# Performance work log

Hardware: AMD Instinct MI355X
Metric: run time of the kernel (lower is better)

The kernel has to match this reference:

```python
import jax, jax.numpy as jnp
import numpy as np

NC = 128      # nc
K = 5         # cube kernel size
NS = 3        # n_scale pyramid levels
NV = 150000   # vertices (cortical-surface scale)
NF = 300000   # faces ~ 2*NV
L = 192       # volume side (L = W = H -> rescale = [1,1,1])


def setup_inputs() -> dict:
    key = jax.random.key(0)
    ks = jax.random.split(key, 16)
    s = 0.05
    return {
        "v": jax.random.uniform(ks[0], (1, NV, 3), minval=-0.9, maxval=0.9, dtype=jnp.float32),
        "f": jax.random.randint(ks[1], (1, NF, 3), 0, NV, dtype=jnp.int32),
        "volume": jax.random.normal(ks[2], (1, 1, L, L, L), dtype=jnp.float32),
        "fc1_w": jax.random.normal(ks[3], (6, NC), dtype=jnp.float32) * s,
        "fc1_b": jnp.zeros((NC,), jnp.float32),
        "fc2_w": jax.random.normal(ks[4], (2 * NC, 4 * NC), dtype=jnp.float32) * s,
        "fc2_b": jnp.zeros((4 * NC,), jnp.float32),
        "fc3_w": jax.random.normal(ks[5], (4 * NC, 2 * NC), dtype=jnp.float32) * s,
        "fc3_b": jnp.zeros((2 * NC,), jnp.float32),
        "fc4_w": jax.random.normal(ks[6], (2 * NC, 3), dtype=jnp.float32) * s,
        "fc4_b": jnp.zeros((3,), jnp.float32),
        "conv_w": jax.random.normal(ks[7], (NC, NS, K, K, K), dtype=jnp.float32) * s,
        "conv_b": jnp.zeros((NC,), jnp.float32),
        "lfc_w": jax.random.normal(ks[8], (NC, NC), dtype=jnp.float32) * s,
        "lfc_b": jnp.zeros((NC,), jnp.float32),
    }


def _vertex_normals(v, f):
    # pytorch3d-style vertex normals: scatter-add area-weighted face normals, then normalize.
    verts, faces = v[0], f[0]
    p0, p1, p2 = verts[faces[:, 0]], verts[faces[:, 1]], verts[faces[:, 2]]
    fn = jnp.cross(p1 - p0, p2 - p0)  # [NF, 3]
    n = jnp.zeros_like(verts)
    n = n.at[faces[:, 0]].add(fn).at[faces[:, 1]].add(fn).at[faces[:, 2]].add(fn)
    n = n / jnp.maximum(jnp.linalg.norm(n, axis=-1, keepdims=True), 1e-12)
    return n[None]  # [1, NV, 3]


def _cube_sampling(v, volume):
    # Vectorized version of the 125-iteration Python gather loop:
    # gather a KxKxK neighborhood per vertex at each pyramid scale.
    vol_n = volume[0, 0]
    off = jnp.arange(-(K - 1) // 2, (K - 1) // 2 + 1)  # [-2..2]
    cubes = []
    for n in range(NS):
        if n > 0:
            s = vol_n.shape[0]
            vol_n = vol_n.reshape(s // 2, 2, s // 2, 2, s // 2, 2).mean(axis=(1, 3, 5))  # avg_pool3d(2)
        idx = jnp.round((v[0] + 1.0) * L / 2 ** (n + 1)).astype(jnp.int32)  # rescale = [1,1,1]
        idx = jnp.clip(idx, (K - 1) // 2, L // 2 ** n - 3)
        i0 = idx[:, 0, None, None, None] + off[None, :, None, None]
        i1 = idx[:, 1, None, None, None] + off[None, None, :, None]
        i2 = idx[:, 2, None, None, None] + off[None, None, None, :]
        cubes.append(vol_n[i0, i1, i2])  # [NV, K, K, K]
    return jnp.stack(cubes, axis=1)  # [NV, NS, K, K, K]


def reference(v, f, volume, fc1_w, fc1_b, fc2_w, fc2_b, fc3_w, fc3_b, fc4_w, fc4_b,
              conv_w, conv_b, lfc_w, lfc_b):
    coord = v
    normal = _vertex_normals(v, f)
    x = jnp.concatenate([v, normal], axis=2)                 # [1, NV, 6]
    x = jax.nn.leaky_relu(x @ fc1_w + fc1_b, 0.15)           # [1, NV, NC]
    cubes = _cube_sampling(v, volume)                        # [NV, NS, K, K, K]
    # Conv3d with kernel == input size -> single output voxel == full contraction.
    x_local = jnp.einsum('ncijk,ocijk->no', cubes, conv_w) + conv_b  # [NV, NC]
    x_local = (x_local @ lfc_w + lfc_b)[None]                # [1, NV, NC]
    x = jnp.concatenate([x, x_local], axis=2)                # [1, NV, 2*NC]
    x = jax.nn.leaky_relu(x @ fc2_w + fc2_b, 0.15)
    x = jax.nn.leaky_relu(x @ fc3_w + fc3_b, 0.15)
    x = jnp.tanh(x @ fc4_w + fc4_b) * 0.1
    return coord + x
```

## Files before the change

### kernel.cpp

```cpp
#include <hip/hip_runtime.h>
#include <hip/hip_bf16.h>
#include <math.h>

#define NVERT 150000
#define NFACE 300000
#define LVOL  192
#define TVB   32
#define MTV   48

#define P2_POOL1 3456
#define P2_POOL2 432
#define P2_WC    193
#define P2_CP0   3456
#define P2_POOL2_START (P2_POOL1)
#define P2_WC_START    (P2_POOL1 + P2_POOL2)
#define P2_CP0_START   (P2_POOL1 + P2_POOL2 + P2_WC)

#define NB_NORM 1172
#define NB_TRS  1024

#define WS_BIG_NEED 44808576ull
#define WS_B16_NEED 58964352ull

typedef short v8s __attribute__((ext_vector_type(8)));
typedef float v4f __attribute__((ext_vector_type(4)));

__device__ __forceinline__ float s2f(short s) {
    unsigned int u = ((unsigned int)(unsigned short)s) << 16;
    return __builtin_bit_cast(float, u);
}
__device__ __forceinline__ short f2s(float f) {
    __hip_bfloat16 h = __float2bfloat16(f);
    return __builtin_bit_cast(short, h);
}
__device__ __forceinline__ float lrelu(float x) { return x > 0.f ? x : 0.15f * x; }

__device__ __forceinline__ float ldf(const void* __restrict__ p, int i, int bf) {
    return bf ? s2f(((const short*)p)[i]) : ((const float*)p)[i];
}

__device__ __forceinline__ int haddr(int r, int c) {
    int hi  = c >> 7;
    int mid = (c >> 4) & 7;
    int lo  = c & 15;
    int wc  = hi * 64 + (mid & 3) * 16 + lo;
    return ((mid < 4) ? 0 : 12672) + r * 264 + wc;
}

__global__ void detect_kernel(const void* __restrict__ v, int* __restrict__ flag) {
    __shared__ int s_ok;
    int t = threadIdx.x;
    if (t == 0) s_ok = 1;
    __syncthreads();
    float x = s2f(((const short*)v)[t]);
    if (!(fabsf(x) <= 1.0f)) atomicAnd(&s_ok, 0);
    __syncthreads();
    if (t == 0) *flag = s_ok;
}

__global__ __launch_bounds__(256) void mega_prep2_kernel(
    const void* __restrict__ volume,
    short* __restrict__ vol1b, short* __restrict__ vol2b,
    const void* __restrict__ conv_w, const void* __restrict__ lfc_w,
    const void* __restrict__ conv_b, const void* __restrict__ lfc_b,
    short* __restrict__ Wcomb, float* __restrict__ bcomb,
    const int* __restrict__ flag,
    short* __restrict__ vol0b)
{
    const int bf = *flag;
    const int bid = blockIdx.x;
    const int t = threadIdx.x;

    if (bid < P2_POOL1) {
        int id = bid * 256 + t;
        int z = id % 96, y = (id / 96) % 96, x = id / (96 * 96);
        float s = 0.f;
        #pragma unroll
        for (int a = 0; a < 2; a++)
            #pragma unroll
            for (int b = 0; b < 2; b++)
                #pragma unroll
                for (int c = 0; c < 2; c++)
                    s += ldf(volume, (2 * x + a) * (LVOL * LVOL) + (2 * y + b) * LVOL + (2 * z + c), bf);
        s *= 0.125f;
        vol1b[id] = f2s(s);
    } else if (bid < P2_WC_START) {
        int id = (bid - P2_POOL2_START) * 256 + t;
        int z = id % 48, y = (id / 48) % 48, x = id / (48 * 48);
        float s = 0.f;
        for (int a = 0; a < 4; a++)
            for (int b = 0; b < 4; b++)
                #pragma unroll
                for (int c = 0; c < 4; c++)
                    s += ldf(volume, (4 * x + a) * (LVOL * LVOL) + (4 * y + b) * LVOL + (4 * z + c), bf);
        s *= 0.015625f;
        vol2b[id] = f2s(s);
    } else if (bid < P2_CP0_START) {
        int id = (bid - P2_WC_START) * 256 + t;
        if (id < 49152) {
            int j = id / 384, k = id - j * 384;
            float acc = 0.f;
            if (k < 375) {
                float a0 = 0.f, a1 = 0.f, a2 = 0.f, a3 = 0.f;
                for (int o = 0; o < 128; o += 4) {
                    a0 += ldf(conv_w, (o + 0) * 375 + k, bf) * ldf(lfc_w, (o + 0) * 128 + j, bf);
                    a1 += ldf(conv_w, (o + 1) * 375 + k, bf) * ldf(lfc_w, (o + 1) * 128 + j, bf);
                    a2 += ldf(conv_w, (o + 2) * 375 + k, bf) * ldf(lfc_w, (o + 2) * 128 + j, bf);
                    a3 += ldf(conv_w, (o + 3) * 375 + k, bf) * ldf(lfc_w, (o + 3) * 128 + j, bf);
                }
                acc = (a0 + a1) + (a2 + a3);
            }
            int tile = j >> 4, ln = j & 15;
            int kk = k >> 5, r = k & 31, qq = r >> 3, e = r & 7;
            Wcomb[((tile * 12 + kk) * 64 + qq * 16 + ln) * 8 + e] = f2s(acc);
        } else if (id < 49152 + 128) {
            int j = id - 49152;
            float acc = ldf(lfc_b, j, bf);
            for (int o = 0; o < 128; o++) acc += ldf(conv_b, o, bf) * ldf(lfc_w, o * 128 + j, bf);
            bcomb[j] = acc;
        }
    } else {
        if (bf) return;
        int id = (bid - P2_CP0_START) * 2048 + t * 8;
        const float* vp = (const float*)volume;
        short tmp[8];
        #pragma unroll
        for (int i = 0; i < 8; i++) tmp[i] = f2s(vp[id + i]);
        *(v8s*)&vol0b[id] = *(v8s*)tmp;
    }
}

__global__ __launch_bounds__(256, 6) void gather_ext_kernel(
    const void* __restrict__ v,
    const int* __restrict__ f, float* __restrict__ n_accum,
    const void* __restrict__ volume,
    const short* __restrict__ vol1b,
    const short* __restrict__ vol2b,
    const short* __restrict__ vol0b,
    const short* __restrict__ Wcomb,
    const float* __restrict__ bcomb,
    const void* __restrict__ fc2_w, const void* __restrict__ fc3_w,
    short* __restrict__ fc2T, short* __restrict__ fc3T,
    short* __restrict__ xloc,
    const int* __restrict__ flag, int ngather)
{
    __shared__ __align__(16) short sCube[TVB * 392];
    __shared__ int sIdx[TVB * 4];

    const int bf = *flag;
    const int t = threadIdx.x;
    const int bid = blockIdx.x;

    if (bid >= ngather) {
        int rb = bid - ngather;
        if (rb < NB_NORM) {
            int ft = rb * 256 + t;
            if (ft >= NFACE) return;
            int i0 = f[ft * 3 + 0], i1 = f[ft * 3 + 1], i2 = f[ft * 3 + 2];
            float p0x = ldf(v, i0 * 3 + 0, bf), p0y = ldf(v, i0 * 3 + 1, bf), p0z = ldf(v, i0 * 3 + 2, bf);
            float p1x = ldf(v, i1 * 3 + 0, bf), p1y = ldf(v, i1 * 3 + 1, bf), p1z = ldf(v, i1 * 3 + 2, bf);
            float p2x = ldf(v, i2 * 3 + 0, bf), p2y = ldf(v, i2 * 3 + 1, bf), p2z = ldf(v, i2 * 3 + 2, bf);
            float e1x = p1x - p0x, e1y = p1y - p0y, e1z = p1z - p0z;
            float e2x = p2x - p0x, e2y = p2y - p0y, e2z = p2z - p0z;
            float cx = e1y * e2z - e1z * e2y;
            float cy = e1z * e2x - e1x * e2z;
            float cz = e1x * e2y - e1y * e2x;
            atomicAdd(&n_accum[i0 * 3 + 0], cx); atomicAdd(&n_accum[i0 * 3 + 1], cy); atomicAdd(&n_accum[i0 * 3 + 2], cz);
            atomicAdd(&n_accum[i1 * 3 + 0], cx); atomicAdd(&n_accum[i1 * 3 + 1], cy); atomicAdd(&n_accum[i1 * 3 + 2], cz);
            atomicAdd(&n_accum[i2 * 3 + 0], cx); atomicAdd(&n_accum[i2 * 3 + 1], cy); atomicAdd(&n_accum[i2 * 3 + 2], cz);
        } else {
            int id = (rb - NB_NORM) * 256 + t;
            if (id < 131072) {
                int col = id >> 8, k = id & 255;
                int tile = col >> 4, ln = col & 15;
                int kk = k >> 5, r = k & 31, qq = r >> 3, e = r & 7;
                fc2T[((tile * 8 + kk) * 64 + qq * 16 + ln) * 8 + e] = f2s(ldf(fc2_w, k * 512 + col, bf));
            } else {
                int i = id - 131072;
                int col = i >> 9, k = i & 511;
                int tile = col >> 4, ln = col & 15;
                int kk = k >> 5, r = k & 31, qq = r >> 3, e = r & 7;
                fc3T[((tile * 16 + kk) * 64 + qq * 16 + ln) * 8 + e] = f2s(ldf(fc3_w, k * 256 + col, bf));
            }
        }
        return;
    }

    const int base = bid * TVB;
    const int w = t >> 6, L = t & 63, q = L >> 4, ln = L & 15;
    const short* v0 = bf ? (const short*)volume : vol0b;

    if (t < TVB) {
        int vert = min(base + t, NVERT - 1);
        float vx = ldf(v, vert * 3 + 0, bf);
        float vy = ldf(v, vert * 3 + 1, bf);
        float vz = ldf(v, vert * 3 + 2, bf);
        #pragma unroll
        for (int n = 0; n < 3; n++) {
            float scl = (n == 0) ? 96.0f : (n == 1 ? 48.0f : 24.0f);
            int dim = LVOL >> n, lim = dim - 3;
            int cx = min(max((int)rintf((vx + 1.0f) * scl), 2), lim);
            int cy = min(max((int)rintf((vy + 1.0f) * scl), 2), lim);
            int cz = min(max((int)rintf((vz + 1.0f) * scl), 2), lim);
            sIdx[t * 4 + n] = (cx * dim + cy) * dim + (cz - 2);
        }
    }
    __syncthreads();

    for (int idx = t; idx < TVB * 75; idx += 256) {
        int n   = idx / 800;
        int rem = idx - n * 800;
        int vl  = rem / 25;
        int dd  = rem - vl * 25;
        int di  = dd / 5, dj = dd - di * 5;
        int dim = LVOL >> n;
        int addr = sIdx[vl * 4 + n] + (di - 2) * dim * dim + (dj - 2) * dim;
        short* dst = &sCube[vl * 392 + n * 125 + dd * 5];
        if (n == 0 && v0 == nullptr) {
            const float* vp = (const float*)volume;
            #pragma unroll
            for (int i = 0; i < 5; i++) dst[i] = f2s(vp[addr + i]);
        } else {
            const short* lvl = (n == 0) ? v0 : (n == 1 ? vol1b : vol2b);
            #pragma unroll
            for (int i = 0; i < 5; i++) dst[i] = lvl[addr + i];
        }
    }
    for (int idx = t; idx < TVB * 9; idx += 256) {
        int vl = idx / 9, rr = idx - vl * 9;
        sCube[vl * 392 + 375 + rr] = 0;
    }
    __syncthreads();

    #pragma unroll
    for (int nt = 0; nt < 2; nt++) {
        int col = w * 32 + nt * 16 + ln;
        const short* wb = Wcomb + ((w * 2 + nt) * 12 * 64 + q * 16 + ln) * 8;
        v4f acc0 = {0.f, 0.f, 0.f, 0.f}, acc1 = {0.f, 0.f, 0.f, 0.f};
        #pragma unroll
        for (int k0 = 0; k0 < 12; k0++) {
            v8s b  = *(const v8s*)(wb + k0 * 512);
            v8s a0 = *(const v8s*)&sCube[ln * 392 + k0 * 32 + q * 8];
            v8s a1 = *(const v8s*)&sCube[(16 + ln) * 392 + k0 * 32 + q * 8];
            acc0 = __builtin_amdgcn_mfma_f32_16x16x32_bf16(a0, b, acc0, 0, 0, 0);
            acc1 = __builtin_amdgcn_mfma_f32_16x16x32_bf16(a1, b, acc1, 0, 0, 0);
        }
        float bias = bcomb[col];
        #pragma unroll
        for (int r = 0; r < 4; r++) {
            xloc[(base + q * 4 + r) * 128 + col]      = f2s(acc0[r] + bias);
            xloc[(base + 16 + q * 4 + r) * 128 + col] = f2s(acc1[r] + bias);
        }
    }
}

__global__ __launch_bounds__(256, 3) void mlp_kernel(
    const void* __restrict__ v,
    const float* __restrict__ n_accum,
    const short* __restrict__ xloc,
    const short* __restrict__ fc2T,
    const short* __restrict__ fc3T,
    const void* __restrict__ fc1_w, const void* __restrict__ fc1_b,
    const void* __restrict__ fc2_b, const void* __restrict__ fc3_b,
    const void* __restrict__ fc4_w, const void* __restrict__ fc4_b,
    void* __restrict__ out,
    const int* __restrict__ flag)
{
    __shared__ __align__(16) char smem[52224];
    short* sX  = (short*)smem;
    short* sHB = (short*)smem;
    short* s3  = (short*)smem;
    short* sW4 = (short*)(smem + 50688);

    const int bf = *flag;
    const int t = threadIdx.x;
    const int base = blockIdx.x * MTV;
    const int w = t >> 6, L = t & 63, q = L >> 4, ln = L & 15;
    const int laneoff = (q * 16 + ln) * 8;

    for (int id = t; id < MTV * 16; id += 256) {
        int row = id >> 4, seg = id & 15;
        v8s x = *(const v8s*)(xloc + (base + row) * 128 + seg * 8);
        *(v8s*)&sX[row * 264 + 128 + seg * 8] = x;
    }

    for (int i = t; i < 768; i += 256) {
        int j = i >> 8, k = i & 255;
        sW4[i] = f2s(ldf(fc4_w, k * 3 + j, bf));
    }

    {
        int vi = t >> 2, cb = (t & 3) * 32;
        if (vi < MTV) {
            int vert = base + vi;
            float i0 = ldf(v, vert * 3 + 0, bf);
            float i1 = ldf(v, vert * 3 + 1, bf);
            float i2 = ldf(v, vert * 3 + 2, bf);
            float nx = n_accum[vert * 3 + 0];
            float ny = n_accum[vert * 3 + 1];
            float nz = n_accum[vert * 3 + 2];
            float inv = 1.0f / fmaxf(sqrtf(nx * nx + ny * ny + nz * nz), 1e-12f);
            float i3 = nx * inv, i4 = ny * inv, i5 = nz * inv;
            #pragma unroll 8
            for (int i = 0; i < 32; i++) {
                int c = cb + i;
                float acc = ldf(fc1_b, c, bf)
                          + i0 * ldf(fc1_w, 0 * 128 + c, bf)
                          + i1 * ldf(fc1_w, 1 * 128 + c, bf)
                          + i2 * ldf(fc1_w, 2 * 128 + c, bf)
                          + i3 * ldf(fc1_w, 3 * 128 + c, bf)
                          + i4 * ldf(fc1_w, 4 * 128 + c, bf)
                          + i5 * ldf(fc1_w, 5 * 128 + c, bf);
                sX[vi * 264 + c] = f2s(lrelu(acc));
            }
        }
    }
    __syncthreads();

    {
        #pragma unroll
        for (int nt = 4; nt < 8; nt++) {
            int col = w * 128 + nt * 16 + ln;
            const short* bb = fc2T + (w * 8 + nt) * 8 * 512 + laneoff;
            v4f acc0 = {0.f, 0.f, 0.f, 0.f}, acc1 = {0.f, 0.f, 0.f, 0.f}, acc2 = {0.f, 0.f, 0.f, 0.f};
            #pragma unroll
            for (int k0 = 0; k0 < 8; k0++) {
                v8s b  = *(const v8s*)(bb + k0 * 512);
                v8s a0 = *(const v8s*)&sX[(ln) * 264 + k0 * 32 + q * 8];
                v8s a1 = *(const v8s*)&sX[(16 + ln) * 264 + k0 * 32 + q * 8];
                v8s a2 = *(const v8s*)&sX[(32 + ln) * 264 + k0 * 32 + q * 8];
                acc0 = __builtin_amdgcn_mfma_f32_16x16x32_bf16(a0, b, acc0, 0, 0, 0);
                acc1 = __builtin_amdgcn_mfma_f32_16x16x32_bf16(a1, b, acc1, 0, 0, 0);
                acc2 = __builtin_amdgcn_mfma_f32_16x16x32_bf16(a2, b, acc2, 0, 0, 0);
            }
            float bias = ldf(fc2_b, col, bf);
            int wc = 12672 + w * 64 + (nt - 4) * 16 + ln;
            #pragma unroll
            for (int r = 0; r < 4; r++) {
                sHB[(q * 4 + r) * 264 + wc]      = f2s(lrelu(acc0[r] + bias));
                sHB[(16 + q * 4 + r) * 264 + wc] = f2s(lrelu(acc1[r] + bias));
                sHB[(32 + q * 4 + r) * 264 + wc] = f2s(lrelu(acc2[r] + bias));
            }
        }

        v4f accL[4][3];
        #pragma unroll
        for (int nt = 0; nt < 4; nt++)
            #pragma unroll
            for (int m = 0; m < 3; m++)
                accL[nt][m] = (v4f){0.f, 0.f, 0.f, 0.f};

        #pragma unroll
        for (int nt = 0; nt < 4; nt++) {
            const short* bb = fc2T + (w * 8 + nt) * 8 * 512 + laneoff;
            #pragma unroll
            for (int k0 = 0; k0 < 8; k0++) {
                v8s b  = *(const v8s*)(bb + k0 * 512);
                v8s a0 = *(const v8s*)&sX[(ln) * 264 + k0 * 32 + q * 8];
                v8s a1 = *(const v8s*)&sX[(16 + ln) * 264 + k0 * 32 + q * 8];
                v8s a2 = *(const v8s*)&sX[(32 + ln) * 264 + k0 * 32 + q * 8];
                accL[nt][0] = __builtin_amdgcn_mfma_f32_16x16x32_bf16(a0, b, accL[nt][0], 0, 0, 0);
                accL[nt][1] = __builtin_amdgcn_mfma_f32_16x16x32_bf16(a1, b, accL[nt][1], 0, 0, 0);
                accL[nt][2] = __builtin_amdgcn_mfma_f32_16x16x32_bf16(a2, b, accL[nt][2], 0, 0, 0);
            }
        }
        __syncthreads();

        #pragma unroll
        for (int nt = 0; nt < 4; nt++) {
            int col = w * 128 + nt * 16 + ln;
            float bias = ldf(fc2_b, col, bf);
            int wc = w * 64 + nt * 16 + ln;
            #pragma unroll
            for (int r = 0; r < 4; r++) {
                sHB[(q * 4 + r) * 264 + wc]      = f2s(lrelu(accL[nt][0][r] + bias));
                sHB[(16 + q * 4 + r) * 264 + wc] = f2s(lrelu(accL[nt][1][r] + bias));
                sHB[(32 + q * 4 + r) * 264 + wc] = f2s(lrelu(accL[nt][2][r] + bias));
            }
        }
    }
    __syncthreads();

    {
        v4f acc[4][3];
        #pragma unroll
        for (int nt = 0; nt < 4; nt++)
            #pragma unroll
            for (int m = 0; m < 3; m++)
                acc[nt][m] = (v4f){0.f, 0.f, 0.f, 0.f};

        #pragma unroll
        for (int half = 0; half < 2; half++) {
            v8s A0[8], A1[8], A2[8];
            #pragma unroll
            for (int k0 = 0; k0 < 8; k0++) {
                int c = half * 256 + k0 * 32 + q * 8;
                A0[k0] = *(const v8s*)&sHB[haddr(ln, c)];
                A1[k0] = *(const v8s*)&sHB[haddr(16 + ln, c)];
                A2[k0] = *(const v8s*)&sHB[haddr(32 + ln, c)];
            }
            #pragma unroll
            for (int nt = 0; nt < 4; nt++) {
                const short* bb = fc3T + ((w * 4 + nt) * 16 + half * 8) * 512 + laneoff;
                v8s B[8];
                #pragma unroll
                for (int k0 = 0; k0 < 8; k0++) B[k0] = *(const v8s*)(bb + k0 * 512);
                #pragma unroll
                for (int k0 = 0; k0 < 8; k0++) {
                    acc[nt][0] = __builtin_amdgcn_mfma_f32_16x16x32_bf16(A0[k0], B[k0], acc[nt][0], 0, 0, 0);
                    acc[nt][1] = __builtin_amdgcn_mfma_f32_16x16x32_bf16(A1[k0], B[k0], acc[nt][1], 0, 0, 0);
                    acc[nt][2] = __builtin_amdgcn_mfma_f32_16x16x32_bf16(A2[k0], B[k0], acc[nt][2], 0, 0, 0);
                }
            }
        }
        __syncthreads();

        #pragma unroll
        for (int nt = 0; nt < 4; nt++) {
            int col = w * 64 + nt * 16 + ln;
            float bias = ldf(fc3_b, col, bf);
            #pragma unroll
            for (int r = 0; r < 4; r++) {
                s3[(q * 4 + r) * 264 + col]      = f2s(lrelu(acc[nt][0][r] + bias));
                s3[(16 + q * 4 + r) * 264 + col] = f2s(lrelu(acc[nt][1][r] + bias));
                s3[(32 + q * 4 + r) * 264 + col] = f2s(lrelu(acc[nt][2][r] + bias));
            }
        }
    }
    __syncthreads();

    {
        int vi = t >> 2, l = t & 3;
        if (vi < MTV) {
            float p0 = 0.f, p1 = 0.f, p2 = 0.f;
            for (int k = l * 8; k < 256; k += 32) {
                #pragma unroll
                for (int j = 0; j < 8; j++) {
                    float a = s2f(s3[vi * 264 + k + j]);
                    p0 += a * s2f(sW4[0 * 256 + k + j]);
                    p1 += a * s2f(sW4[1 * 256 + k + j]);
                    p2 += a * s2f(sW4[2 * 256 + k + j]);
                }
            }
            #pragma unroll
            for (int s = 2; s; s >>= 1) {
                p0 += __shfl_down(p0, s, 4);
                p1 += __shfl_down(p1, s, 4);
                p2 += __shfl_down(p2, s, 4);
            }
            if (l == 0) {
                int vert = base + vi;
                float vx = ldf(v, vert * 3 + 0, bf);
                float vy = ldf(v, vert * 3 + 1, bf);
                float vz = ldf(v, vert * 3 + 2, bf);
                float o0 = vx + 0.1f * tanhf(p0 + ldf(fc4_b, 0, bf));
                float o1 = vy + 0.1f * tanhf(p1 + ldf(fc4_b, 1, bf));
                float o2 = vz + 0.1f * tanhf(p2 + ldf(fc4_b, 2, bf));
                if (bf) {
                    short* ob = (short*)out;
                    ob[vert * 3 + 0] = f2s(o0);
                    ob[vert * 3 + 1] = f2s(o1);
                    ob[vert * 3 + 2] = f2s(o2);
                } else {
                    float* of = (float*)out;
                    of[vert * 3 + 0] = o0;
                    of[vert * 3 + 1] = o1;
                    of[vert * 3 + 2] = o2;
                }
            }
        }
    }
}

__global__ __launch_bounds__(256, 3) void fused_mfma_kernel(
    const void* __restrict__ v,
    const float* __restrict__ n_accum,
    const void* __restrict__ volume,
    const short* __restrict__ vol1,
    const short* __restrict__ vol2,
    const short* __restrict__ Wcomb,
    const float* __restrict__ bcomb,
    const short* __restrict__ fc2T,
    const short* __restrict__ fc3T,
    const void* __restrict__ fc1_w, const void* __restrict__ fc1_b,
    const void* __restrict__ fc2_b, const void* __restrict__ fc3_b,
    const void* __restrict__ fc4_w, const void* __restrict__ fc4_b,
    void* __restrict__ out,
    const int* __restrict__ flag)
{
    __shared__ __align__(16) char smem[51712];
    short* sX    = (short*)smem;
    short* sCube = (short*)(smem + 16896);
    short* sH    = (short*)(smem + 16896);
    short* s3    = (short*)smem;
    short* sW4   = (short*)(smem + 50176);

    const int bf = *flag;
    const int t = threadIdx.x;
    const int base = blockIdx.x * TVB;
    const int w = t >> 6, L = t & 63, q = L >> 4, ln = L & 15;
    const int laneoff = (q * 16 + ln) * 8;

    for (int idx = t; idx < TVB * 75; idx += 256) {
        int vl  = idx / 75;
        int r75 = idx - vl * 75;
        int n   = r75 / 25;
        int dd  = r75 - n * 25;
        int di  = dd / 5, dj = dd - di * 5;
        int vert = base + vl;
        short* dst = &sCube[vl * 392 + n * 125 + dd * 5];
        if (vert < NVERT) {
            float vx = ldf(v, vert * 3 + 0, bf);
            float vy = ldf(v, vert * 3 + 1, bf);
            float vz = ldf(v, vert * 3 + 2, bf);
            float scl = (n == 0) ? 96.0f : (n == 1 ? 48.0f : 24.0f);
            int lim = (LVOL >> n) - 3;
            int cx = (int)rintf((vx + 1.0f) * scl);
            int cy = (int)rintf((vy + 1.0f) * scl);
            int cz = (int)rintf((vz + 1.0f) * scl);
            cx = min(max(cx, 2), lim) + di - 2;
            cy = min(max(cy, 2), lim) + dj - 2;
            cz = min(max(cz, 2), lim);
            if (n == 0) {
                int b0 = (cx * LVOL + cy) * LVOL + (cz - 2);
                if (bf) {
                    const short* vp = (const short*)volume;
                    #pragma unroll
                    for (int i = 0; i < 5; i++) dst[i] = vp[b0 + i];
                } else {
                    const float* vp = (const float*)volume;
                    #pragma unroll
                    for (int i = 0; i < 5; i++) dst[i] = f2s(vp[b0 + i]);
                }
            } else {
                const short* lvl = (n == 1) ? vol1 : vol2;
                int dim = (n == 1) ? 96 : 48;
                int b0 = (cx * dim + cy) * dim + (cz - 2);
                #pragma unroll
                for (int i = 0; i < 5; i++) dst[i] = lvl[b0 + i];
            }
        } else {
            #pragma unroll
            for (int i = 0; i < 5; i++) dst[i] = 0;
        }
    }
    for (int idx = t; idx < TVB * 9; idx += 256) {
        int vl = idx / 9, rr = idx - vl * 9;
        sCube[vl * 392 + 375 + rr] = 0;
    }
    for (int i = t; i < 768; i += 256) {
        int j = i >> 8, k = i & 255;
        sW4[i] = f2s(ldf(fc4_w, k * 3 + j, bf));
    }
    {
        int vi = t & 31, cb = (t >> 5) * 16;
        int vert = base + vi;
        float i0 = 0.f, i1 = 0.f, i2 = 0.f, i3 = 0.f, i4 = 0.f, i5 = 0.f;
        if (vert < NVERT) {
            i0 = ldf(v, vert * 3 + 0, bf);
            i1 = ldf(v, vert * 3 + 1, bf);
            i2 = ldf(v, vert * 3 + 2, bf);
            float nx = n_accum[vert * 3 + 0];
            float ny = n_accum[vert * 3 + 1];
            float nz = n_accum[vert * 3 + 2];
            float inv = 1.0f / fmaxf(sqrtf(nx * nx + ny * ny + nz * nz), 1e-12f);
            i3 = nx * inv; i4 = ny * inv; i5 = nz * inv;
        }
        #pragma unroll
        for (int i = 0; i < 16; i++) {
            int c = cb + i;
            float acc = ldf(fc1_b, c, bf)
                      + i0 * ldf(fc1_w, 0 * 128 + c, bf)
                      + i1 * ldf(fc1_w, 1 * 128 + c, bf)
                      + i2 * ldf(fc1_w, 2 * 128 + c, bf)
                      + i3 * ldf(fc1_w, 3 * 128 + c, bf)
                      + i4 * ldf(fc1_w, 4 * 128 + c, bf)
                      + i5 * ldf(fc1_w, 5 * 128 + c, bf);
            sX[vi * 264 + c] = f2s(lrelu(acc));
        }
    }
    __syncthreads();

    #pragma unroll
    for (int nt = 0; nt < 2; nt++) {
        int col = w * 32 + nt * 16 + ln;
        const short* wb = Wcomb + ((w * 2 + nt) * 12 * 64) * 8 + laneoff;
        v4f acc0 = {0.f, 0.f, 0.f, 0.f}, acc1 = {0.f, 0.f, 0.f, 0.f};
        #pragma unroll
        for (int k0 = 0; k0 < 12; k0++) {
            v8s b  = *(const v8s*)(wb + k0 * 512);
            v8s a0 = *(const v8s*)&sCube[ln * 392 + k0 * 32 + q * 8];
            v8s a1 = *(const v8s*)&sCube[(16 + ln) * 392 + k0 * 32 + q * 8];
            acc0 = __builtin_amdgcn_mfma_f32_16x16x32_bf16(a0, b, acc0, 0, 0, 0);
            acc1 = __builtin_amdgcn_mfma_f32_16x16x32_bf16(a1, b, acc1, 0, 0, 0);
        }
        float bias = bcomb[col];
        #pragma unroll
        for (int r = 0; r < 4; r++) {
            sX[(q * 4 + r) * 264 + 128 + col]      = f2s(acc0[r] + bias);
            sX[(16 + q * 4 + r) * 264 + 128 + col] = f2s(acc1[r] + bias);
        }
    }
    __syncthreads();

    {
        v8s a0[8], a1[8];
        #pragma unroll
        for (int k0 = 0; k0 < 8; k0++) {
            a0[k0] = *(const v8s*)&sX[ln * 264 + k0 * 32 + q * 8];
            a1[k0] = *(const v8s*)&sX[(16 + ln) * 264 + k0 * 32 + q * 8];
        }
        #pragma unroll
        for (int nt = 0; nt < 8; nt++) {
            int col = w * 128 + nt * 16 + ln;
            const short* bb = fc2T + (w * 8 + nt) * 8 * 512 + laneoff;
            v4f acc0 = {0.f, 0.f, 0.f, 0.f}, acc1 = {0.f, 0.f, 0.f, 0.f};
            #pragma unroll
            for (int k0 = 0; k0 < 8; k0++) {
                v8s b = *(const v8s*)(bb + k0 * 512);
                acc0 = __builtin_amdgcn_mfma_f32_16x16x32_bf16(a0[k0], b, acc0, 0, 0, 0);
                acc1 = __builtin_amdgcn_mfma_f32_16x16x32_bf16(a1[k0], b, acc1, 0, 0, 0);
            }
            float bias = ldf(fc2_b, col, bf);
            #pragma unroll
            for (int r = 0; r < 4; r++) {
                sH[(q * 4 + r) * 520 + col]      = f2s(lrelu(acc0[r] + bias));
                sH[(16 + q * 4 + r) * 520 + col] = f2s(lrelu(acc1[r] + bias));
            }
        }
    }
    __syncthreads();

    {
        #pragma unroll
        for (int nt = 0; nt < 4; nt++) {
            int col = w * 64 + nt * 16 + ln;
            v4f acc0 = {0.f, 0.f, 0.f, 0.f}, acc1 = {0.f, 0.f, 0.f, 0.f};
            #pragma unroll
            for (int half = 0; half < 2; half++) {
                const short* bb = fc3T + ((w * 4 + nt) * 16 + half * 8) * 512 + laneoff;
                #pragma unroll
                for (int k0 = 0; k0 < 8; k0++) {
                    v8s b  = *(const v8s*)(bb + k0 * 512);
                    v8s a0 = *(const v8s*)&sH[ln * 520 + half * 256 + k0 * 32 + q * 8];
                    v8s a1 = *(const v8s*)&sH[(16 + ln) * 520 + half * 256 + k0 * 32 + q * 8];
                    acc0 = __builtin_amdgcn_mfma_f32_16x16x32_bf16(a0, b, acc0, 0, 0, 0);
                    acc1 = __builtin_amdgcn_mfma_f32_16x16x32_bf16(a1, b, acc1, 0, 0, 0);
                }
            }
            float bias = ldf(fc3_b, col, bf);
            #pragma unroll
            for (int r = 0; r < 4; r++) {
                s3[(q * 4 + r) * 264 + col]      = f2s(lrelu(acc0[r] + bias));
                s3[(16 + q * 4 + r) * 264 + col] = f2s(lrelu(acc1[r] + bias));
            }
        }
    }
    __syncthreads();

    {
        int vi = t >> 3, l = t & 7;
        float p0 = 0.f, p1 = 0.f, p2 = 0.f;
        for (int k = l; k < 256; k += 8) {
            float a = s2f(s3[vi * 264 + k]);
            p0 += a * s2f(sW4[0 * 256 + k]);
            p1 += a * s2f(sW4[1 * 256 + k]);
            p2 += a * s2f(sW4[2 * 256 + k]);
        }
        #pragma unroll
        for (int s = 4; s; s >>= 1) {
            p0 += __shfl_down(p0, s, 8);
            p1 += __shfl_down(p1, s, 8);
            p2 += __shfl_down(p2, s, 8);
        }
        if (l == 0) {
            int vert = base + vi;
            if (vert < NVERT) {
                float vx = ldf(v, vert * 3 + 0, bf);
                float vy = ldf(v, vert * 3 + 1, bf);
                float vz = ldf(v, vert * 3 + 2, bf);
                float o0 = vx + 0.1f * tanhf(p0 + ldf(fc4_b, 0, bf));
                float o1 = vy + 0.1f * tanhf(p1 + ldf(fc4_b, 1, bf));
                float o2 = vz + 0.1f * tanhf(p2 + ldf(fc4_b, 2, bf));
                if (bf) {
                    short* ob = (short*)out;
                    ob[vert * 3 + 0] = f2s(o0);
                    ob[vert * 3 + 1] = f2s(o1);
                    ob[vert * 3 + 2] = f2s(o2);
                } else {
                    float* of = (float*)out;
                    of[vert * 3 + 0] = o0;
                    of[vert * 3 + 1] = o1;
                    of[vert * 3 + 2] = o2;
                }
            }
        }
    }
}

extern "C" void kernel_launch(void* const* d_in, const int* in_sizes, int n_in,
                              void* d_out, int out_size, void* d_ws, size_t ws_size,
                              hipStream_t stream) {
    const void* v      = d_in[0];
    const int*  f      = (const int*)d_in[1];
    const void* volume = d_in[2];
    const void* fc1_w  = d_in[3];
    const void* fc1_b  = d_in[4];
    const void* fc2_w  = d_in[5];
    const void* fc2_b  = d_in[6];
    const void* fc3_w  = d_in[7];
    const void* fc3_b  = d_in[8];
    const void* fc4_w  = d_in[9];
    const void* fc4_b  = d_in[10];
    const void* conv_w = d_in[11];
    const void* conv_b = d_in[12];
    const void* lfc_w  = d_in[13];
    const void* lfc_b  = d_in[14];

    char* wsb = (char*)d_ws;
    const int big = (ws_size >= WS_BIG_NEED) ? 1 : 0;
    const int b16 = (ws_size >= WS_B16_NEED) ? 1 : 0;

    if (big) {
        int*   flag    = (int*)wsb;
        float* n_accum = (float*)(wsb + 64);
        short* vol1b   = (short*)(wsb + 1800064);
        short* vol2b   = (short*)(wsb + 5339008);
        short* Wcomb   = (short*)(wsb + 5781376);
        float* bcomb   = (float*)(wsb + 5879680);
        short* fc2T    = (short*)(wsb + 5880192);
        short* fc3T    = (short*)(wsb + 6142336);
        short* xloc    = (short*)(wsb + 6404480);
        short* vol0b   = b16 ? (short*)(wsb + 44808576) : nullptr;

        hipMemsetAsync(n_accum, 0, NVERT * 3 * sizeof(float), stream);
        detect_kernel<<<1, 256, 0, stream>>>(v, flag);
        mega_prep2_kernel<<<P2_CP0_START + (b16 ? P2_CP0 : 0), 256, 0, stream>>>(
            volume, vol1b, vol2b,
            conv_w, lfc_w, conv_b, lfc_b, Wcomb, bcomb, flag, vol0b);
        int ngather = (NVERT + TVB - 1) / TVB;
        gather_ext_kernel<<<ngather + NB_NORM + NB_TRS, 256, 0, stream>>>(
            v, f, n_accum, volume, vol1b, vol2b, vol0b, Wcomb, bcomb,
            fc2_w, fc3_w, fc2T, fc3T, xloc, flag, ngather);
        mlp_kernel<<<(NVERT + MTV - 1) / MTV, 256, 0, stream>>>(
            v, n_accum, xloc, fc2T, fc3T,
            fc1_w, fc1_b, fc2_b, fc3_b, fc4_w, fc4_b, d_out, flag);
    } else {
        int*   flag    = (int*)wsb;
        float* n_accum = (float*)(wsb + 64);
        short* vol1    = (short*)(wsb + 1800064);
        short* vol2    = (short*)(wsb + 3569536);
        short* Wcomb   = (short*)(wsb + 3790720);
        float* bcomb   = (float*)(wsb + 3889024);
        short* fc2T    = (short*)(wsb + 3889536);
        short* fc3T    = (short*)(wsb + 4151680);

        hipMemsetAsync(n_accum, 0, NVERT * 3 * sizeof(float), stream);
        detect_kernel<<<1, 256, 0, stream>>>(v, flag);
        mega_prep2_kernel<<<P2_CP0_START, 256, 0, stream>>>(
            volume, vol1, vol2,
            conv_w, lfc_w, conv_b, lfc_b, Wcomb, bcomb, flag, nullptr);
        gather_ext_kernel<<<NB_NORM + NB_TRS, 256, 0, stream>>>(
            v, f, n_accum, volume, vol1, vol2, nullptr, Wcomb, bcomb,
            fc2_w, fc3_w, fc2T, fc3T, nullptr, flag, 0);
        fused_mfma_kernel<<<(NVERT + TVB - 1) / TVB, 256, 0, stream>>>(
            v, n_accum, volume, vol1, vol2, Wcomb, bcomb, fc2T, fc3T,
            fc1_w, fc1_b, fc2_b, fc3_b, fc4_w, fc4_b, d_out, flag);
    }
}
```

Measured before the change: 534.0 us.

## Bucket-sort vertices spatially before cube gather for volume locality

Adds a counting sort (histogram, single-block scan, atomic scatter) that groups vertices by their 8^3-voxel spatial bucket. The gather kernel then processes vertices in this sorted order and scatters its xloc results back to the original vertex rows. The intent is better cache locality for the random 5x5x5 volume gathers across the three pyramid levels. In exchange it adds three extra kernel launches plus a memset, and the xloc writes become scattered rows instead of contiguous ones.

```diff
diff --git a/kernel.cpp b/kernel.cpp
--- a/kernel.cpp
+++ b/kernel.cpp
@@ -19,8 +19,10 @@
 #define NB_NORM 1172
 #define NB_TRS  1024
 
-#define WS_BIG_NEED 44808576ull
-#define WS_B16_NEED 58964352ull
+#define NBUCKET 13824
+#define WS_BIG_NEED  44808576ull
+#define WS_B16_NEED  58964352ull
+#define WS_SORT_NEED 60219648ull
 
 typedef short v8s __attribute__((ext_vector_type(8)));
 typedef float v4f __attribute__((ext_vector_type(4)));
@@ -56,6 +58,64 @@
     if (!(fabsf(x) <= 1.0f)) atomicAnd(&s_ok, 0);
     __syncthreads();
     if (t == 0) *flag = s_ok;
+}
+
+__global__ __launch_bounds__(256) void sort_hist_kernel(
+    const void* __restrict__ v, int* __restrict__ hist, int* __restrict__ keys,
+    const int* __restrict__ flag)
+{
+    const int bf = *flag;
+    int vert = blockIdx.x * 256 + threadIdx.x;
+    if (vert >= NVERT) return;
+    float vx = ldf(v, vert * 3 + 0, bf);
+    float vy = ldf(v, vert * 3 + 1, bf);
+    float vz = ldf(v, vert * 3 + 2, bf);
+    int cx = min(max((int)rintf((vx + 1.0f) * 96.0f), 2), 189);
+    int cy = min(max((int)rintf((vy + 1.0f) * 96.0f), 2), 189);
+    int cz = min(max((int)rintf((vz + 1.0f) * 96.0f), 2), 189);
+    int key = ((cx >> 3) * 24 + (cy >> 3)) * 24 + (cz >> 3);
+    keys[vert] = key;
+    atomicAdd(&hist[key], 1);
+}
+
+__global__ __launch_bounds__(1024) void sort_scan_kernel(int* __restrict__ hist)
+{
+    __shared__ int partial[1024];
+    const int t = threadIdx.x;
+    const int CH = 14;
+    int base = t * CH;
+    int sum = 0;
+    #pragma unroll
+    for (int i = 0; i < CH; i++) {
+        int idx = base + i;
+        if (idx < NBUCKET) sum += hist[idx];
+    }
+    partial[t] = sum;
+    __syncthreads();
+    for (int off = 1; off < 1024; off <<= 1) {
+        int x = (t >= off) ? partial[t - off] : 0;
+        __syncthreads();
+        partial[t] += x;
+        __syncthreads();
+    }
+    int run = partial[t] - sum;
+    for (int i = 0; i < CH; i++) {
+        int idx = base + i;
+        if (idx < NBUCKET) {
+            int c = hist[idx];
+            hist[idx] = run;
+            run += c;
+        }
+    }
+}
+
+__global__ __launch_bounds__(256) void sort_scatter_kernel(
+    int* __restrict__ cursor, const int* __restrict__ keys, int* __restrict__ perm)
+{
+    int vert = blockIdx.x * 256 + threadIdx.x;
+    if (vert >= NVERT) return;
+    int pos = atomicAdd(&cursor[keys[vert]], 1);
+    perm[pos] = vert;
 }
 
 __global__ __launch_bounds__(256) void mega_prep2_kernel(
@@ -137,6 +197,7 @@
     const short* __restrict__ vol1b,
     const short* __restrict__ vol2b,
     const short* __restrict__ vol0b,
+    const int* __restrict__ perm,
     const short* __restrict__ Wcomb,
     const float* __restrict__ bcomb,
     const void* __restrict__ fc2_w, const void* __restrict__ fc3_w,
@@ -191,7 +252,8 @@
     const short* v0 = bf ? (const short*)volume : vol0b;
 
     if (t < TVB) {
-        int vert = min(base + t, NVERT - 1);
+        int slot = min(base + t, NVERT - 1);
+        int vert = perm ? perm[slot] : slot;
         float vx = ldf(v, vert * 3 + 0, bf);
         float vy = ldf(v, vert * 3 + 1, bf);
         float vz = ldf(v, vert * 3 + 2, bf);
@@ -204,6 +266,7 @@
             int cz = min(max((int)rintf((vz + 1.0f) * scl), 2), lim);
             sIdx[t * 4 + n] = (cx * dim + cy) * dim + (cz - 2);
         }
+        sIdx[t * 4 + 3] = vert;
     }
     __syncthreads();
 
@@ -248,8 +311,8 @@
         float bias = bcomb[col];
         #pragma unroll
         for (int r = 0; r < 4; r++) {
-            xloc[(base + q * 4 + r) * 128 + col]      = f2s(acc0[r] + bias);
-            xloc[(base + 16 + q * 4 + r) * 128 + col] = f2s(acc1[r] + bias);
+            xloc[sIdx[(q * 4 + r) * 4 + 3] * 128 + col]      = f2s(acc0[r] + bias);
+            xloc[sIdx[(16 + q * 4 + r) * 4 + 3] * 128 + col] = f2s(acc1[r] + bias);
         }
     }
 }
@@ -718,8 +781,9 @@
     const void* lfc_b  = d_in[14];
 
     char* wsb = (char*)d_ws;
-    const int big = (ws_size >= WS_BIG_NEED) ? 1 : 0;
-    const int b16 = (ws_size >= WS_B16_NEED) ? 1 : 0;
+    const int big  = (ws_size >= WS_BIG_NEED) ? 1 : 0;
+    const int b16  = (ws_size >= WS_B16_NEED) ? 1 : 0;
+    const int srt  = (ws_size >= WS_SORT_NEED) ? 1 : 0;
 
     if (big) {
         int*   flag    = (int*)wsb;
@@ -732,15 +796,24 @@
         short* fc3T    = (short*)(wsb + 6142336);
         short* xloc    = (short*)(wsb + 6404480);
         short* vol0b   = b16 ? (short*)(wsb + 44808576) : nullptr;
+        int*   hist    = srt ? (int*)(wsb + 58964352) : nullptr;
+        int*   keys    = srt ? (int*)(wsb + 59019648) : nullptr;
+        int*   perm    = srt ? (int*)(wsb + 59619648) : nullptr;
 
         hipMemsetAsync(n_accum, 0, NVERT * 3 * sizeof(float), stream);
         detect_kernel<<<1, 256, 0, stream>>>(v, flag);
+        if (srt) {
+            hipMemsetAsync(hist, 0, NBUCKET * sizeof(int), stream);
+            sort_hist_kernel<<<(NVERT + 255) / 256, 256, 0, stream>>>(v, hist, keys, flag);
+            sort_scan_kernel<<<1, 1024, 0, stream>>>(hist);
+            sort_scatter_kernel<<<(NVERT + 255) / 256, 256, 0, stream>>>(hist, keys, perm);
+        }
         mega_prep2_kernel<<<P2_CP0_START + (b16 ? P2_CP0 : 0), 256, 0, stream>>>(
             volume, vol1b, vol2b,
             conv_w, lfc_w, conv_b, lfc_b, Wcomb, bcomb, flag, vol0b);
         int ngather = (NVERT + TVB - 1) / TVB;
         gather_ext_kernel<<<ngather + NB_NORM + NB_TRS, 256, 0, stream>>>(
-            v, f, n_accum, volume, vol1b, vol2b, vol0b, Wcomb, bcomb,
+            v, f, n_accum, volume, vol1b, vol2b, vol0b, perm, Wcomb, bcomb,
             fc2_w, fc3_w, fc2T, fc3T, xloc, flag, ngather);
         mlp_kernel<<<(NVERT + MTV - 1) / MTV, 256, 0, stream>>>(
             v, n_accum, xloc, fc2T, fc3T,
@@ -761,7 +834,7 @@
             volume, vol1, vol2,
             conv_w, lfc_w, conv_b, lfc_b, Wcomb, bcomb, flag, nullptr);
         gather_ext_kernel<<<NB_NORM + NB_TRS, 256, 0, stream>>>(
-            v, f, n_accum, volume, vol1, vol2, nullptr, Wcomb, bcomb,
+            v, f, n_accum, volume, vol1, vol2, nullptr, nullptr, Wcomb, bcomb,
             fc2_w, fc3_w, fc2T, fc3T, nullptr, flag, 0);
         fused_mfma_kernel<<<(NVERT + TVB - 1) / TVB, 256, 0, stream>>>(
             v, n_accum, volume, vol1, vol2, Wcomb, bcomb, fc2T, fc3T,
```

New measurement: 531.6 us. No clear change (-0.4%).
